# Optimization experiments

Hardware: AMD Instinct MI355X
Metric: run time of the kernel (lower is better)

## Reference

```python
import jax, jax.numpy as jnp
import numpy as np

B, H, S, D = 4, 16, 2048, 128

def setup_inputs() -> dict:
    key = jax.random.key(0)
    kq, kk, kv = jax.random.split(key, 3)
    query = jax.random.normal(kq, (B, H, S, D), dtype=jnp.float32)
    k = jax.random.normal(kk, (B, H, S, D), dtype=jnp.float32)
    v = jax.random.normal(kv, (B, H, S, D), dtype=jnp.float32)
    # causal mask: True = masked (not attended), broadcastable to (B,H,S,S)
    mask = jnp.triu(jnp.ones((S, S), dtype=bool), k=1)[None, None, :, :]
    return {"query": query, "key": k, "value": v, "mask": mask}

def reference(query, key, value, mask):
    d_k = query.shape[-1]
    scale = 1.0 / np.sqrt(d_k).astype(np.float32)
    # scores: (B,H,Sq,Sk)
    scores = jnp.einsum('bhqd,bhkd->bhqk', query, key) * scale
    scores = jnp.where(mask, -jnp.inf, scores)
    attention_weights = jax.nn.softmax(scores, axis=-1)
    output = jnp.einsum('bhqk,bhkd->bhqd', attention_weights, value)
    return output, attention_weights
```

## Files before the change

### kernel.cpp

```cpp
#include <hip/hip_runtime.h>
#include <hip/hip_bf16.h>

#define B_ 4
#define H_ 16
#define S_ 2048
#define D_ 128

typedef unsigned short u16;
typedef unsigned int u32;

typedef __attribute__((ext_vector_type(8))) short bf16x8;
typedef __attribute__((ext_vector_type(4))) float f32x4;
typedef __attribute__((ext_vector_type(4))) unsigned short u16x4;

__device__ __forceinline__ float bf2f(u16 x) {
    return __uint_as_float(((u32)x) << 16);
}

__device__ __forceinline__ u16 f2bf(float f) {
    u32 u = __float_as_uint(f);
    u32 lsb = (u >> 16) & 1u;
    u += 0x7fffu + lsb;
    return (u16)(u >> 16);
}

__global__ void detect_dtype_kernel(const u32* __restrict__ q, int* __restrict__ flag) {
    __shared__ int cnt;
    if (threadIdx.x == 0) cnt = 0;
    __syncthreads();
    int c = 0;
    for (int i = threadIdx.x; i < 4096; i += 256) {
        float lo = bf2f((u16)(q[i] & 0xffffu));
        if (!(fabsf(lo) <= 64.0f)) c++;
    }
    atomicAdd(&cnt, c);
    __syncthreads();
    if (threadIdx.x == 0) *flag = (cnt > 256) ? 1 : 0;
}

__global__ __launch_bounds__(256) void attn_bf16_kernel(
    const u16* __restrict__ Q, const u16* __restrict__ K, const u16* __restrict__ V,
    u16* __restrict__ Out, u16* __restrict__ W, const int* __restrict__ flag)
{
    if (*flag != 0) return;

    __shared__ float qs[D_];
    __shared__ float sc[S_];
    __shared__ float red[8];
    __shared__ float ot[512];

    const int tid = threadIdx.x;
    for (int idx = blockIdx.x; idx < B_ * H_ * S_; idx += (int)gridDim.x) {
        const int q   = idx & (S_ - 1);
        const int bh  = idx >> 11;
        const size_t rowQ = (size_t)idx * D_;
        const u16* Kb = K + (size_t)bh * S_ * D_;
        const u16* Vb = V + (size_t)bh * S_ * D_;
        const int nk = q + 1;
        const float scale = 0.08838834764831845f;

        if (tid < D_) qs[tid] = bf2f(Q[rowQ + tid]) * scale;
        __syncthreads();

        float lmax = -1e30f;
        for (int k = tid; k < nk; k += 256) {
            const uint4* K4 = reinterpret_cast<const uint4*>(Kb + (size_t)k * D_);
            float acc = 0.f;
            #pragma unroll
            for (int c = 0; c < D_ / 8; ++c) {
                uint4 u = K4[c];
                const int d = c * 8;
                acc += qs[d + 0] * bf2f((u16)(u.x & 0xffffu));
                acc += qs[d + 1] * bf2f((u16)(u.x >> 16));
                acc += qs[d + 2] * bf2f((u16)(u.y & 0xffffu));
                acc += qs[d + 3] * bf2f((u16)(u.y >> 16));
                acc += qs[d + 4] * bf2f((u16)(u.z & 0xffffu));
                acc += qs[d + 5] * bf2f((u16)(u.z >> 16));
                acc += qs[d + 6] * bf2f((u16)(u.w & 0xffffu));
                acc += qs[d + 7] * bf2f((u16)(u.w >> 16));
            }
            sc[k] = acc;
            lmax = fmaxf(lmax, acc);
        }

        #pragma unroll
        for (int off = 32; off > 0; off >>= 1)
            lmax = fmaxf(lmax, __shfl_down(lmax, off, 64));
        if ((tid & 63) == 0) red[tid >> 6] = lmax;
        __syncthreads();
        const float mx = fmaxf(fmaxf(red[0], red[1]), fmaxf(red[2], red[3]));

        float lsum = 0.f;
        for (int k = tid; k < nk; k += 256) {
            float e = __expf(sc[k] - mx);
            sc[k] = e;
            lsum += e;
        }
        #pragma unroll
        for (int off = 32; off > 0; off >>= 1)
            lsum += __shfl_down(lsum, off, 64);
        if ((tid & 63) == 0) red[4 + (tid >> 6)] = lsum;
        __syncthreads();
        const float rsum = 1.0f / (red[4] + red[5] + red[6] + red[7]);

        u32* Wrow2 = reinterpret_cast<u32*>(W + (size_t)idx * S_);
        for (int k2 = tid; k2 < S_ / 2; k2 += 256) {
            const int k0 = 2 * k2, k1 = 2 * k2 + 1;
            float w0 = (k0 < nk) ? sc[k0] * rsum : 0.f;
            float w1 = (k1 < nk) ? sc[k1] * rsum : 0.f;
            if (k0 < nk) sc[k0] = w0;
            if (k1 < nk) sc[k1] = w1;
            Wrow2[k2] = (u32)f2bf(w0) | ((u32)f2bf(w1) << 16);
        }
        __syncthreads();

        const int d2   = tid & 63;
        const int part = tid >> 6;
        const u32* V2 = reinterpret_cast<const u32*>(Vb);
        float a0 = 0.f, a1 = 0.f;
        for (int k = part; k < nk; k += 4) {
            const u32 u = V2[(size_t)k * (D_ / 2) + d2];
            const float w = sc[k];
            a0 += w * bf2f((u16)(u & 0xffffu));
            a1 += w * bf2f((u16)(u >> 16));
        }
        ot[part * D_ + 2 * d2]     = a0;
        ot[part * D_ + 2 * d2 + 1] = a1;
        __syncthreads();

        if (tid < D_) {
            const float o = ot[tid] + ot[D_ + tid] + ot[2 * D_ + tid] + ot[3 * D_ + tid];
            Out[rowQ + tid] = f2bf(o);
        }
        __syncthreads();
    }
}

__global__ __launch_bounds__(256) void split_qk_kernel(
    const float* __restrict__ Q, const float* __restrict__ K,
    u16* __restrict__ Qh, u16* __restrict__ Ql,
    u16* __restrict__ Kh, u16* __restrict__ Kl,
    const int* __restrict__ flag)
{
    if (*flag != 1) return;
    const float scale = 0.08838834764831845f;
    const int N4 = (B_ * H_ * S_ * D_) / 4;
    const float4* Q4 = reinterpret_cast<const float4*>(Q);
    const float4* K4 = reinterpret_cast<const float4*>(K);
    for (int g = blockIdx.x * 256 + threadIdx.x; g < N4; g += 2048 * 256) {
        {
            float4 v = Q4[g];
            float s0 = v.x * scale, s1 = v.y * scale, s2 = v.z * scale, s3 = v.w * scale;
            u16 h0 = f2bf(s0), h1 = f2bf(s1), h2 = f2bf(s2), h3 = f2bf(s3);
            u16x4 hv = {h0, h1, h2, h3};
            u16x4 lv = {f2bf(s0 - bf2f(h0)), f2bf(s1 - bf2f(h1)),
                        f2bf(s2 - bf2f(h2)), f2bf(s3 - bf2f(h3))};
            *reinterpret_cast<u16x4*>(&Qh[(size_t)4 * g]) = hv;
            *reinterpret_cast<u16x4*>(&Ql[(size_t)4 * g]) = lv;
        }
        {
            float4 v = K4[g];
            u16 h0 = f2bf(v.x), h1 = f2bf(v.y), h2 = f2bf(v.z), h3 = f2bf(v.w);
            u16x4 hv = {h0, h1, h2, h3};
            u16x4 lv = {f2bf(v.x - bf2f(h0)), f2bf(v.y - bf2f(h1)),
                        f2bf(v.z - bf2f(h2)), f2bf(v.w - bf2f(h3))};
            *reinterpret_cast<u16x4*>(&Kh[(size_t)4 * g]) = hv;
            *reinterpret_cast<u16x4*>(&Kl[(size_t)4 * g]) = lv;
        }
    }
}

__global__ __launch_bounds__(256) void transpose_v_kernel(
    const float* __restrict__ V, u16* __restrict__ VT, const int* __restrict__ flag)
{
    if (*flag != 1) return;
    __shared__ float ts[64 * 130];
    const int tid = threadIdx.x;
    const int bh = blockIdx.x >> 5;
    const int kt = blockIdx.x & 31;
    const int k0 = kt * 64;
    const float4* V4 = reinterpret_cast<const float4*>(V + ((size_t)bh * S_ + k0) * D_);
    #pragma unroll
    for (int it = 0; it < 8; ++it) {
        int g = tid + 256 * it;
        int r = g >> 5, c4 = g & 31;
        float4 v = V4[g];
        ts[r * 130 + 4 * c4 + 0] = v.x;
        ts[r * 130 + 4 * c4 + 1] = v.y;
        ts[r * 130 + 4 * c4 + 2] = v.z;
        ts[r * 130 + 4 * c4 + 3] = v.w;
    }
    __syncthreads();
    const int d = tid >> 1, kh2 = tid & 1;
    u16* dst = VT + (size_t)bh * (D_ * S_) + (size_t)d * S_ + k0 + 32 * kh2;
    #pragma unroll
    for (int jj = 0; jj < 4; ++jj) {
        bf16x8 o;
        #pragma unroll
        for (int j = 0; j < 8; ++j) {
            int k = 32 * kh2 + 8 * jj + j;
            o[j] = (short)f2bf(ts[k * 130 + d]);
        }
        *reinterpret_cast<bf16x8*>(&dst[8 * jj]) = o;
    }
}

#define ESTR 68

__global__ __launch_bounds__(256, 2) void attn_mfma_kernel(
    const u16* __restrict__ Qh, const u16* __restrict__ Ql,
    const u16* __restrict__ Kh, const u16* __restrict__ Kl,
    const u16* __restrict__ VT,
    float* __restrict__ Out, float* __restrict__ W, const int* __restrict__ flag)
{
    if (*flag != 1) return;

    __shared__ __align__(16) short qh_s[32 * 128];
    __shared__ __align__(16) short ql_s[32 * 128];
    __shared__ __align__(16) short kh_s[64 * 128];
    __shared__ __align__(16) short kl_s[64 * 128];
    __shared__ __align__(16) short vt_s[128 * 64];
    __shared__ __align__(16) float e_s[32 * ESTR];
    __shared__ float red2[2][32];
    __shared__ float rinv_s[32];

    const int tid = threadIdx.x;
    const int w   = tid >> 6;
    const int l   = tid & 63;
    const int l15 = l & 15;
    const int l4  = l >> 4;
    const int fq  = w >> 1;
    const int fk  = w & 1;

    const int bidx = blockIdx.x;
    const int bh   = bidx >> 6;
    const int qt   = 63 - (bidx & 63);
    const int q0   = qt << 5;
    const int nkt  = (q0 + 95) >> 6;

    const u16* QhB = Qh + ((size_t)bh * S_ + q0) * D_;
    const u16* QlB = Ql + ((size_t)bh * S_ + q0) * D_;
    const u16* KhB = Kh + (size_t)bh * S_ * D_;
    const u16* KlB = Kl + (size_t)bh * S_ * D_;
    const u16* VTB = VT + (size_t)bh * (size_t)D_ * S_;
    float* Ob = Out + ((size_t)bh * S_ + q0) * D_;
    float* Wb = W + ((size_t)bh * S_ + q0) * (size_t)S_;

    #pragma unroll
    for (int it = 0; it < 2; ++it) {
        int g = tid + 256 * it;
        int r = g >> 4, ch = g & 15;
        bf16x8 a = *reinterpret_cast<const bf16x8*>(&QhB[(size_t)r * D_ + 8 * ch]);
        bf16x8 b = *reinterpret_cast<const bf16x8*>(&QlB[(size_t)r * D_ + 8 * ch]);
        int li = r * 128 + ((8 * ch) ^ ((r & 7) << 3));
        *reinterpret_cast<bf16x8*>(&qh_s[li]) = a;
        *reinterpret_cast<bf16x8*>(&ql_s[li]) = b;
    }

    const int qrow = 16 * fq + l15;
    const int qx   = (qrow & 7) << 3;
    const int col0 = 8 * l4;

    f32x4 oacc[4];
    #pragma unroll
    for (int nb = 0; nb < 4; ++nb) { oacc[nb] = {0.f, 0.f, 0.f, 0.f}; }
    float rs[4] = {0.f, 0.f, 0.f, 0.f};

    bf16x8 rkh[4], rkl[4], rvt[4];
    {
        #pragma unroll
        for (int it = 0; it < 4; ++it) {
            int g = tid + 256 * it;
            rkh[it] = *reinterpret_cast<const bf16x8*>(&KhB[(size_t)(g >> 4) * D_ + 8 * (g & 15)]);
            rkl[it] = *reinterpret_cast<const bf16x8*>(&KlB[(size_t)(g >> 4) * D_ + 8 * (g & 15)]);
            rvt[it] = *reinterpret_cast<const bf16x8*>(&VTB[(size_t)(g >> 3) * S_ + 8 * (g & 7)]);
        }
    }

    for (int kt = 0; kt < nkt; ++kt) {
        const int k0 = kt << 6;

        #pragma unroll
        for (int it = 0; it < 4; ++it) {
            int g = tid + 256 * it;
            int r = g >> 4, ch = g & 15;
            int li = r * 128 + ((8 * ch) ^ ((r & 7) << 3));
            *reinterpret_cast<bf16x8*>(&kh_s[li]) = rkh[it];
            *reinterpret_cast<bf16x8*>(&kl_s[li]) = rkl[it];
            int d = g >> 3, c8 = g & 7;
            *reinterpret_cast<bf16x8*>(&vt_s[d * 64 + 8 * (c8 ^ (d & 7))]) = rvt[it];
        }
        __syncthreads();

        if (kt + 1 < nkt) {
            const int kn = k0 + 64;
            #pragma unroll
            for (int it = 0; it < 4; ++it) {
                int g = tid + 256 * it;
                rkh[it] = *reinterpret_cast<const bf16x8*>(&KhB[(size_t)(kn + (g >> 4)) * D_ + 8 * (g & 15)]);
                rkl[it] = *reinterpret_cast<const bf16x8*>(&KlB[(size_t)(kn + (g >> 4)) * D_ + 8 * (g & 15)]);
                rvt[it] = *reinterpret_cast<const bf16x8*>(&VTB[(size_t)(g >> 3) * S_ + kn + 8 * (g & 7)]);
            }
        }

        f32x4 acc2[2];
        acc2[0] = {0.f, 0.f, 0.f, 0.f};
        acc2[1] = {0.f, 0.f, 0.f, 0.f};
        #pragma unroll
        for (int nb = 0; nb < 2; ++nb) {
            const int krow = 32 * fk + 16 * nb + l15;
            const int kx   = (krow & 7) << 3;
            #pragma unroll
            for (int ks = 0; ks < 4; ++ks) {
                int ca = 32 * ks + col0;
                bf16x8 aH = *reinterpret_cast<const bf16x8*>(&qh_s[qrow * 128 + (ca ^ qx)]);
                bf16x8 aL = *reinterpret_cast<const bf16x8*>(&ql_s[qrow * 128 + (ca ^ qx)]);
                bf16x8 bH = *reinterpret_cast<const bf16x8*>(&kh_s[krow * 128 + (ca ^ kx)]);
                bf16x8 bL = *reinterpret_cast<const bf16x8*>(&kl_s[krow * 128 + (ca ^ kx)]);
                acc2[nb] = __builtin_amdgcn_mfma_f32_16x16x32_bf16(aH, bH, acc2[nb], 0, 0, 0);
                acc2[nb] = __builtin_amdgcn_mfma_f32_16x16x32_bf16(aH, bL, acc2[nb], 0, 0, 0);
                acc2[nb] = __builtin_amdgcn_mfma_f32_16x16x32_bf16(aL, bH, acc2[nb], 0, 0, 0);
            }
        }

        #pragma unroll
        for (int nb = 0; nb < 2; ++nb) {
            #pragma unroll
            for (int i = 0; i < 4; ++i) {
                int row = 16 * fq + 4 * l4 + i;
                int col = 32 * fk + 16 * nb + l15;
                float e = 0.f;
                if (k0 + col <= q0 + row) e = __expf(acc2[nb][i]);
                rs[i] += e;
                e_s[row * ESTR + col] = e;
            }
        }
        __syncthreads();

        #pragma unroll
        for (int t = 0; t < 2; ++t) {
            int idx = tid + 256 * t;
            int row = idx >> 4, c4 = idx & 15;
            f32x4 wv = *reinterpret_cast<const f32x4*>(&e_s[row * ESTR + 4 * c4]);
            *reinterpret_cast<f32x4*>(Wb + (size_t)row * S_ + k0 + 4 * c4) = wv;
        }

        #pragma unroll
        for (int ks2 = 0; ks2 < 2; ++ks2) {
            bf16x8 aP;
            {
                const float* pr = &e_s[(16 * fq + l15) * ESTR + 32 * ks2 + col0];
                float4 p0 = *reinterpret_cast<const float4*>(pr);
                float4 p1 = *reinterpret_cast<const float4*>(pr + 4);
                aP[0] = (short)f2bf(p0.x); aP[1] = (short)f2bf(p0.y);
                aP[2] = (short)f2bf(p0.z); aP[3] = (short)f2bf(p0.w);
                aP[4] = (short)f2bf(p1.x); aP[5] = (short)f2bf(p1.y);
                aP[6] = (short)f2bf(p1.z); aP[7] = (short)f2bf(p1.w);
            }
            #pragma unroll
            for (int nb = 0; nb < 4; ++nb) {
                int dcol = 64 * fk + 16 * nb + l15;
                bf16x8 bV = *reinterpret_cast<const bf16x8*>(
                    &vt_s[dcol * 64 + 8 * ((4 * ks2 + l4) ^ (dcol & 7))]);
                oacc[nb] = __builtin_amdgcn_mfma_f32_16x16x32_bf16(aP, bV, oacc[nb], 0, 0, 0);
            }
        }
        __syncthreads();
    }

    #pragma unroll
    for (int i = 0; i < 4; ++i) {
        float v = rs[i];
        v += __shfl_xor(v, 1, 64);
        v += __shfl_xor(v, 2, 64);
        v += __shfl_xor(v, 4, 64);
        v += __shfl_xor(v, 8, 64);
        if (l15 == 0) red2[fk][16 * fq + 4 * l4 + i] = v;
    }
    __syncthreads();
    if (tid < 32) rinv_s[tid] = 1.0f / (red2[0][tid] + red2[1][tid]);
    __syncthreads();

    #pragma unroll
    for (int nb = 0; nb < 4; ++nb) {
        #pragma unroll
        for (int i = 0; i < 4; ++i) {
            int row = 16 * fq + 4 * l4 + i;
            int col = 64 * fk + 16 * nb + l15;
            Ob[(size_t)row * D_ + col] = oacc[nb][i] * rinv_s[row];
        }
    }

    {
        const int kend = nkt << 6;
        f32x4* W4 = reinterpret_cast<f32x4*>(Wb);
        const f32x4 z4 = {0.f, 0.f, 0.f, 0.f};
        for (int g = tid; g < 32 * (S_ / 4); g += 256) {
            const int row = g >> 9;
            const int c4  = g & 511;
            const size_t off = (size_t)row * (S_ / 4) + c4;
            if ((c4 << 2) < kend) {
                f32x4 wv = W4[off];
                const float inv = rinv_s[row];
                wv.x *= inv; wv.y *= inv; wv.z *= inv; wv.w *= inv;
                W4[off] = wv;
            } else {
                __builtin_nontemporal_store(z4, &W4[off]);
            }
        }
    }
}

#define BQ 32
#define BK 64
#define LSTR 33
#define FESTR 68

__device__ __forceinline__ void dot4(float& a, const float4& x, const float4& y) {
    a = fmaf(x.x, y.x, a); a = fmaf(x.y, y.y, a);
    a = fmaf(x.z, y.z, a); a = fmaf(x.w, y.w, a);
}
__device__ __forceinline__ void fma4(float4& a, float s, const float4& b) {
    a.x = fmaf(s, b.x, a.x); a.y = fmaf(s, b.y, a.y);
    a.z = fmaf(s, b.z, a.z); a.w = fmaf(s, b.w, a.w);
}

__global__ __launch_bounds__(256) void attn_f32_tiled(
    const float* __restrict__ Q, const float* __restrict__ K, const float* __restrict__ V,
    float* __restrict__ Out, float* __restrict__ W, const int* __restrict__ flag)
{
    if (*flag != 1) return;

    __shared__ float4 qs4[BQ * LSTR];
    __shared__ float4 kv4[BK * LSTR];
    __shared__ __align__(16) float e_s[BQ * FESTR];
    __shared__ float rsum_s[BQ];
    __shared__ float rinv_s[BQ];

    const int tid  = threadIdx.x;
    const int bidx = blockIdx.x;
    const int bh   = bidx >> 6;
    const int qt   = 63 - (bidx & 63);
    const int q0   = qt << 5;
    const int nkt  = ((q0 + BQ - 1) >> 6) + 1;
    const float scale = 0.08838834764831845f;

    const float* Kb = K + (size_t)bh * (S_ * D_);
    const float* Vb = V + (size_t)bh * (S_ * D_);
    const float* Qb = Q + ((size_t)bh * S_ + q0) * D_;
    float* Ob = Out + ((size_t)bh * S_ + q0) * D_;
    float* Wb = W + ((size_t)bh * S_ + q0) * (size_t)S_;

    const int rgq = tid >> 4;
    const int cgq = tid & 15;
    const int rg = tid >> 4;
    const int cg = tid & 15;

    {
        const float4* Qg = reinterpret_cast<const float4*>(Qb);
        #pragma unroll
        for (int t = 0; t < 4; ++t) {
            const int g = tid + 256 * t;
            qs4[(g >> 5) * LSTR + (g & 31)] = Qg[g];
        }
        const float4* Kg = reinterpret_cast<const float4*>(Kb);
        #pragma unroll
        for (int t = 0; t < 8; ++t) {
            const int g = tid + 256 * t;
            kv4[(g >> 5) * LSTR + (g & 31)] = Kg[g];
        }
    }
    __syncthreads();

    float4 o4[2][2] = {};
    float rsf[2] = {0.f, 0.f};

    for (int kt = 0; kt < nkt; ++kt) {
        const int k0 = kt << 6;
        const bool more = (kt + 1 < nkt);

        float4 vreg[8];
        {
            const float4* Vg = reinterpret_cast<const float4*>(Vb) + (size_t)k0 * 32;
            #pragma unroll
            for (int t = 0; t < 8; ++t) vreg[t] = Vg[tid + 256 * t];
        }

        float acc[2][4] = {};
        {
            const int qb0 = (rgq * 2 + 0) * LSTR;
            const int qb1 = (rgq * 2 + 1) * LSTR;
            const int kb0 = (cgq +  0) * LSTR;
            const int kb1 = (cgq + 16) * LSTR;
            const int kb2 = (cgq + 32) * LSTR;
            const int kb3 = (cgq + 48) * LSTR;
            #pragma unroll 4
            for (int d4 = 0; d4 < 32; ++d4) {
                const float4 qv0 = qs4[qb0 + d4];
                const float4 qv1 = qs4[qb1 + d4];
                const float4 kv0 = kv4[kb0 + d4];
                const float4 kv1 = kv4[kb1 + d4];
                const float4 kv2 = kv4[kb2 + d4];
                const float4 kv3 = kv4[kb3 + d4];
                dot4(acc[0][0], qv0, kv0); dot4(acc[0][1], qv0, kv1);
                dot4(acc[0][2], qv0, kv2); dot4(acc[0][3], qv0, kv3);
                dot4(acc[1][0], qv1, kv0); dot4(acc[1][1], qv1, kv1);
                dot4(acc[1][2], qv1, kv2); dot4(acc[1][3], qv1, kv3);
            }
        }

        #pragma unroll
        for (int i = 0; i < 2; ++i) {
            const int r  = rgq * 2 + i;
            const int qg = q0 + r;
            float* Wrow = Wb + (size_t)r * S_ + k0;
            #pragma unroll
            for (int j = 0; j < 4; ++j) {
                const int kc = cgq + 16 * j;
                const float e = (k0 + kc <= qg) ? __expf(acc[i][j] * scale) : 0.0f;
                rsf[i] += e;
                e_s[r * FESTR + kc] = e;
                Wrow[kc] = e;
            }
        }
        __syncthreads();

        #pragma unroll
        for (int t = 0; t < 8; ++t) {
            const int g = tid + 256 * t;
            kv4[(g >> 5) * LSTR + (g & 31)] = vreg[t];
        }
        float4 kreg[8];
        if (more) {
            const float4* Kg = reinterpret_cast<const float4*>(Kb) + (size_t)(k0 + BK) * 32;
            #pragma unroll
            for (int t = 0; t < 8; ++t) kreg[t] = Kg[tid + 256 * t];
        }
        __syncthreads();

        {
            const int eb0 = (rg * 2 + 0) * FESTR;
            const int eb1 = (rg * 2 + 1) * FESTR;
            #pragma unroll 2
            for (int kk = 0; kk < BK; kk += 4) {
                const float4 e0 = *reinterpret_cast<const float4*>(&e_s[eb0 + kk]);
                const float4 e1 = *reinterpret_cast<const float4*>(&e_s[eb1 + kk]);
                const float ea[4] = {e0.x, e0.y, e0.z, e0.w};
                const float eb[4] = {e1.x, e1.y, e1.z, e1.w};
                #pragma unroll
                for (int t = 0; t < 4; ++t) {
                    const float4 v0 = kv4[(kk + t) * LSTR + cg];
                    const float4 v1 = kv4[(kk + t) * LSTR + 16 + cg];
                    fma4(o4[0][0], ea[t], v0);
                    fma4(o4[0][1], ea[t], v1);
                    fma4(o4[1][0], eb[t], v0);
                    fma4(o4[1][1], eb[t], v1);
                }
            }
        }

        if (more) {
            __syncthreads();
            #pragma unroll
            for (int t = 0; t < 8; ++t) {
                const int g = tid + 256 * t;
                kv4[(g >> 5) * LSTR + (g & 31)] = kreg[t];
            }
            __syncthreads();
        }
    }

    #pragma unroll
    for (int i = 0; i < 2; ++i) {
        float v = rsf[i];
        v += __shfl_xor(v, 8, 64);
        v += __shfl_xor(v, 4, 64);
        v += __shfl_xor(v, 2, 64);
        v += __shfl_xor(v, 1, 64);
        if (cgq == 0) rsum_s[rgq * 2 + i] = v;
    }
    __syncthreads();
    if (tid < BQ) rinv_s[tid] = 1.0f / rsum_s[tid];
    __syncthreads();

    #pragma unroll
    for (int i = 0; i < 2; ++i) {
        const int r = rg * 2 + i;
        const float inv = rinv_s[r];
        float4 a = o4[i][0];
        a.x *= inv; a.y *= inv; a.z *= inv; a.w *= inv;
        float4 b = o4[i][1];
        b.x *= inv; b.y *= inv; b.z *= inv; b.w *= inv;
        float4* Orow = reinterpret_cast<float4*>(Ob + (size_t)r * D_);
        Orow[cg]      = a;
        Orow[16 + cg] = b;
    }

    {
        const int kend = nkt << 6;
        float4* W4 = reinterpret_cast<float4*>(Wb);
        for (int g = tid; g < BQ * (S_ / 4); g += 256) {
            const int row = g >> 9;
            const int c4  = g & 511;
            const size_t off = (size_t)row * (S_ / 4) + c4;
            if ((c4 << 2) < kend) {
                float4 wv = W4[off];
                const float inv = rinv_s[row];
                wv.x *= inv; wv.y *= inv; wv.z *= inv; wv.w *= inv;
                W4[off] = wv;
            } else {
                W4[off] = make_float4(0.f, 0.f, 0.f, 0.f);
            }
        }
    }
}

extern "C" void kernel_launch(void* const* d_in, const int* in_sizes, int n_in,
                              void* d_out, int out_size, void* d_ws, size_t ws_size,
                              hipStream_t stream) {
    int* flag = (int*)d_ws;

    detect_dtype_kernel<<<dim3(1), dim3(256), 0, stream>>>((const u32*)d_in[0], flag);

    {
        const u16* Q = (const u16*)d_in[0];
        const u16* K = (const u16*)d_in[1];
        const u16* V = (const u16*)d_in[2];
        u16* Out = (u16*)d_out;
        u16* Wp  = Out + (size_t)B_ * H_ * S_ * D_;
        attn_bf16_kernel<<<dim3(2048), dim3(256), 0, stream>>>(Q, K, V, Out, Wp, flag);
    }

    const size_t PLSZ = (size_t)B_ * H_ * S_ * D_;
    const size_t NEED = 256 + 5 * PLSZ * sizeof(u16);
    float* OutF = (float*)d_out;
    float* WF   = OutF + PLSZ;

    if (ws_size >= NEED) {
        u16* base = (u16*)((char*)d_ws + 256);
        u16* Qh = base;
        u16* Ql = Qh + PLSZ;
        u16* Kh = Ql + PLSZ;
        u16* Kl = Kh + PLSZ;
        u16* VTp = Kl + PLSZ;
        split_qk_kernel<<<dim3(2048), dim3(256), 0, stream>>>(
            (const float*)d_in[0], (const float*)d_in[1], Qh, Ql, Kh, Kl, flag);
        transpose_v_kernel<<<dim3(2048), dim3(256), 0, stream>>>(
            (const float*)d_in[2], VTp, flag);
        attn_mfma_kernel<<<dim3(B_ * H_ * (S_ / 32)), dim3(256), 0, stream>>>(
            Qh, Ql, Kh, Kl, VTp, OutF, WF, flag);
    } else {
        attn_f32_tiled<<<dim3(B_ * H_ * (S_ / 32)), dim3(256), 0, stream>>>(
            (const float*)d_in[0], (const float*)d_in[1], (const float*)d_in[2],
            OutF, WF, flag);
    }
}
```

Before: 1.918 ms.

## Make each wave own 16 query rows and read K/V directly from global

Each 256-thread block now covers 64 query rows, and each wave independently handles 16 of them. Q fragments are held in registers, and K and V^T fragments are loaded straight from global memory (relying on cache) instead of being staged cooperatively through shared memory. Per-wave shared memory is used only for the exp tile, so block-wide __syncthreads are removed and LDS use drops sharply. In exchange, the four waves each fetch the same K/V tiles from global/L2 without sharing, and the prefetch double-buffering is gone. The launch grid is halved to match the larger query tile.

```diff
diff --git a/kernel.cpp b/kernel.cpp
--- a/kernel.cpp
+++ b/kernel.cpp
@@ -215,141 +215,90 @@
 {
     if (*flag != 1) return;
 
-    __shared__ __align__(16) short qh_s[32 * 128];
-    __shared__ __align__(16) short ql_s[32 * 128];
-    __shared__ __align__(16) short kh_s[64 * 128];
-    __shared__ __align__(16) short kl_s[64 * 128];
-    __shared__ __align__(16) short vt_s[128 * 64];
-    __shared__ __align__(16) float e_s[32 * ESTR];
-    __shared__ float red2[2][32];
-    __shared__ float rinv_s[32];
+    __shared__ __align__(16) float e_s[4][16 * ESTR];
 
     const int tid = threadIdx.x;
-    const int w   = tid >> 6;
+    const int wv  = tid >> 6;
     const int l   = tid & 63;
     const int l15 = l & 15;
     const int l4  = l >> 4;
-    const int fq  = w >> 1;
-    const int fk  = w & 1;
 
     const int bidx = blockIdx.x;
-    const int bh   = bidx >> 6;
-    const int qt   = 63 - (bidx & 63);
-    const int q0   = qt << 5;
-    const int nkt  = (q0 + 95) >> 6;
-
-    const u16* QhB = Qh + ((size_t)bh * S_ + q0) * D_;
-    const u16* QlB = Ql + ((size_t)bh * S_ + q0) * D_;
+    const int bh   = bidx >> 5;
+    const int qt   = 31 - (bidx & 31);
+    const int q0   = qt << 6;
+    const int nkt  = qt + 1;
+    const int qw   = q0 + 16 * wv;
+
+    const u16* QhW = Qh + ((size_t)bh * S_ + qw) * D_;
+    const u16* QlW = Ql + ((size_t)bh * S_ + qw) * D_;
     const u16* KhB = Kh + (size_t)bh * S_ * D_;
     const u16* KlB = Kl + (size_t)bh * S_ * D_;
     const u16* VTB = VT + (size_t)bh * (size_t)D_ * S_;
-    float* Ob = Out + ((size_t)bh * S_ + q0) * D_;
-    float* Wb = W + ((size_t)bh * S_ + q0) * (size_t)S_;
-
-    #pragma unroll
-    for (int it = 0; it < 2; ++it) {
-        int g = tid + 256 * it;
-        int r = g >> 4, ch = g & 15;
-        bf16x8 a = *reinterpret_cast<const bf16x8*>(&QhB[(size_t)r * D_ + 8 * ch]);
-        bf16x8 b = *reinterpret_cast<const bf16x8*>(&QlB[(size_t)r * D_ + 8 * ch]);
-        int li = r * 128 + ((8 * ch) ^ ((r & 7) << 3));
-        *reinterpret_cast<bf16x8*>(&qh_s[li]) = a;
-        *reinterpret_cast<bf16x8*>(&ql_s[li]) = b;
-    }
-
-    const int qrow = 16 * fq + l15;
-    const int qx   = (qrow & 7) << 3;
-    const int col0 = 8 * l4;
-
-    f32x4 oacc[4];
-    #pragma unroll
-    for (int nb = 0; nb < 4; ++nb) { oacc[nb] = {0.f, 0.f, 0.f, 0.f}; }
+    float* Ob = Out + ((size_t)bh * S_ + qw) * D_;
+    float* Wb = W + ((size_t)bh * S_ + qw) * (size_t)S_;
+
+    float* ew = e_s[wv];
+
+    bf16x8 aH[4], aL[4];
+    #pragma unroll
+    for (int ks = 0; ks < 4; ++ks) {
+        aH[ks] = *reinterpret_cast<const bf16x8*>(&QhW[(size_t)l15 * D_ + 32 * ks + 8 * l4]);
+        aL[ks] = *reinterpret_cast<const bf16x8*>(&QlW[(size_t)l15 * D_ + 32 * ks + 8 * l4]);
+    }
+
+    f32x4 oacc[8];
+    #pragma unroll
+    for (int nb = 0; nb < 8; ++nb) { oacc[nb] = {0.f, 0.f, 0.f, 0.f}; }
     float rs[4] = {0.f, 0.f, 0.f, 0.f};
-
-    bf16x8 rkh[4], rkl[4], rvt[4];
-    {
-        #pragma unroll
-        for (int it = 0; it < 4; ++it) {
-            int g = tid + 256 * it;
-            rkh[it] = *reinterpret_cast<const bf16x8*>(&KhB[(size_t)(g >> 4) * D_ + 8 * (g & 15)]);
-            rkl[it] = *reinterpret_cast<const bf16x8*>(&KlB[(size_t)(g >> 4) * D_ + 8 * (g & 15)]);
-            rvt[it] = *reinterpret_cast<const bf16x8*>(&VTB[(size_t)(g >> 3) * S_ + 8 * (g & 7)]);
-        }
-    }
 
     for (int kt = 0; kt < nkt; ++kt) {
         const int k0 = kt << 6;
 
-        #pragma unroll
-        for (int it = 0; it < 4; ++it) {
-            int g = tid + 256 * it;
-            int r = g >> 4, ch = g & 15;
-            int li = r * 128 + ((8 * ch) ^ ((r & 7) << 3));
-            *reinterpret_cast<bf16x8*>(&kh_s[li]) = rkh[it];
-            *reinterpret_cast<bf16x8*>(&kl_s[li]) = rkl[it];
-            int d = g >> 3, c8 = g & 7;
-            *reinterpret_cast<bf16x8*>(&vt_s[d * 64 + 8 * (c8 ^ (d & 7))]) = rvt[it];
-        }
-        __syncthreads();
-
-        if (kt + 1 < nkt) {
-            const int kn = k0 + 64;
-            #pragma unroll
-            for (int it = 0; it < 4; ++it) {
-                int g = tid + 256 * it;
-                rkh[it] = *reinterpret_cast<const bf16x8*>(&KhB[(size_t)(kn + (g >> 4)) * D_ + 8 * (g & 15)]);
-                rkl[it] = *reinterpret_cast<const bf16x8*>(&KlB[(size_t)(kn + (g >> 4)) * D_ + 8 * (g & 15)]);
-                rvt[it] = *reinterpret_cast<const bf16x8*>(&VTB[(size_t)(g >> 3) * S_ + kn + 8 * (g & 7)]);
-            }
-        }
-
-        f32x4 acc2[2];
-        acc2[0] = {0.f, 0.f, 0.f, 0.f};
-        acc2[1] = {0.f, 0.f, 0.f, 0.f};
-        #pragma unroll
-        for (int nb = 0; nb < 2; ++nb) {
-            const int krow = 32 * fk + 16 * nb + l15;
-            const int kx   = (krow & 7) << 3;
+        f32x4 sc[4];
+        #pragma unroll
+        for (int nb = 0; nb < 4; ++nb) {
+            const u16* khp = KhB + (size_t)(k0 + 16 * nb + l15) * D_ + 8 * l4;
+            const u16* klp = KlB + (size_t)(k0 + 16 * nb + l15) * D_ + 8 * l4;
+            f32x4 accA = {0.f, 0.f, 0.f, 0.f};
+            f32x4 accB = {0.f, 0.f, 0.f, 0.f};
             #pragma unroll
             for (int ks = 0; ks < 4; ++ks) {
-                int ca = 32 * ks + col0;
-                bf16x8 aH = *reinterpret_cast<const bf16x8*>(&qh_s[qrow * 128 + (ca ^ qx)]);
-                bf16x8 aL = *reinterpret_cast<const bf16x8*>(&ql_s[qrow * 128 + (ca ^ qx)]);
-                bf16x8 bH = *reinterpret_cast<const bf16x8*>(&kh_s[krow * 128 + (ca ^ kx)]);
-                bf16x8 bL = *reinterpret_cast<const bf16x8*>(&kl_s[krow * 128 + (ca ^ kx)]);
-                acc2[nb] = __builtin_amdgcn_mfma_f32_16x16x32_bf16(aH, bH, acc2[nb], 0, 0, 0);
-                acc2[nb] = __builtin_amdgcn_mfma_f32_16x16x32_bf16(aH, bL, acc2[nb], 0, 0, 0);
-                acc2[nb] = __builtin_amdgcn_mfma_f32_16x16x32_bf16(aL, bH, acc2[nb], 0, 0, 0);
-            }
-        }
-
-        #pragma unroll
-        for (int nb = 0; nb < 2; ++nb) {
+                bf16x8 bH = *reinterpret_cast<const bf16x8*>(khp + 32 * ks);
+                bf16x8 bL = *reinterpret_cast<const bf16x8*>(klp + 32 * ks);
+                accA = __builtin_amdgcn_mfma_f32_16x16x32_bf16(aH[ks], bH, accA, 0, 0, 0);
+                accB = __builtin_amdgcn_mfma_f32_16x16x32_bf16(aH[ks], bL, accB, 0, 0, 0);
+                accB = __builtin_amdgcn_mfma_f32_16x16x32_bf16(aL[ks], bH, accB, 0, 0, 0);
+            }
+            sc[nb] = accA + accB;
+        }
+
+        #pragma unroll
+        for (int nb = 0; nb < 4; ++nb) {
             #pragma unroll
             for (int i = 0; i < 4; ++i) {
-                int row = 16 * fq + 4 * l4 + i;
-                int col = 32 * fk + 16 * nb + l15;
+                const int row  = 4 * l4 + i;
+                const int colg = k0 + 16 * nb + l15;
                 float e = 0.f;
-                if (k0 + col <= q0 + row) e = __expf(acc2[nb][i]);
+                if (colg <= qw + row) e = __expf(sc[nb][i]);
                 rs[i] += e;
-                e_s[row * ESTR + col] = e;
-            }
-        }
-        __syncthreads();
-
-        #pragma unroll
-        for (int t = 0; t < 2; ++t) {
-            int idx = tid + 256 * t;
-            int row = idx >> 4, c4 = idx & 15;
-            f32x4 wv = *reinterpret_cast<const f32x4*>(&e_s[row * ESTR + 4 * c4]);
-            *reinterpret_cast<f32x4*>(Wb + (size_t)row * S_ + k0 + 4 * c4) = wv;
+                ew[row * ESTR + 16 * nb + l15] = e;
+            }
+        }
+
+        #pragma unroll
+        for (int t = 0; t < 4; ++t) {
+            const int g = t * 64 + l;
+            const int r = g >> 4, c4 = g & 15;
+            f32x4 wvv = *reinterpret_cast<const f32x4*>(&ew[r * ESTR + 4 * c4]);
+            *reinterpret_cast<f32x4*>(Wb + (size_t)r * S_ + k0 + 4 * c4) = wvv;
         }
 
         #pragma unroll
         for (int ks2 = 0; ks2 < 2; ++ks2) {
             bf16x8 aP;
             {
-                const float* pr = &e_s[(16 * fq + l15) * ESTR + 32 * ks2 + col0];
+                const float* pr = &ew[l15 * ESTR + 32 * ks2 + 8 * l4];
                 float4 p0 = *reinterpret_cast<const float4*>(pr);
                 float4 p1 = *reinterpret_cast<const float4*>(pr + 4);
                 aP[0] = (short)f2bf(p0.x); aP[1] = (short)f2bf(p0.y);
@@ -358,16 +307,15 @@
                 aP[6] = (short)f2bf(p1.z); aP[7] = (short)f2bf(p1.w);
             }
             #pragma unroll
-            for (int nb = 0; nb < 4; ++nb) {
-                int dcol = 64 * fk + 16 * nb + l15;
-                bf16x8 bV = *reinterpret_cast<const bf16x8*>(
-                    &vt_s[dcol * 64 + 8 * ((4 * ks2 + l4) ^ (dcol & 7))]);
-                oacc[nb] = __builtin_amdgcn_mfma_f32_16x16x32_bf16(aP, bV, oacc[nb], 0, 0, 0);
-            }
-        }
-        __syncthreads();
-    }
-
+            for (int nb2 = 0; nb2 < 8; ++nb2) {
+                const u16* vp = VTB + (size_t)(16 * nb2 + l15) * S_ + k0 + 32 * ks2 + 8 * l4;
+                bf16x8 bV = *reinterpret_cast<const bf16x8*>(vp);
+                oacc[nb2] = __builtin_amdgcn_mfma_f32_16x16x32_bf16(aP, bV, oacc[nb2], 0, 0, 0);
+            }
+        }
+    }
+
+    float rinv[4];
     #pragma unroll
     for (int i = 0; i < 4; ++i) {
         float v = rs[i];
@@ -375,37 +323,37 @@
         v += __shfl_xor(v, 2, 64);
         v += __shfl_xor(v, 4, 64);
         v += __shfl_xor(v, 8, 64);
-        if (l15 == 0) red2[fk][16 * fq + 4 * l4 + i] = v;
-    }
-    __syncthreads();
-    if (tid < 32) rinv_s[tid] = 1.0f / (red2[0][tid] + red2[1][tid]);
-    __syncthreads();
-
-    #pragma unroll
-    for (int nb = 0; nb < 4; ++nb) {
+        rinv[i] = 1.0f / v;
+        ew[(4 * l4 + i) * ESTR + 64] = rinv[i];
+    }
+
+    #pragma unroll
+    for (int nb2 = 0; nb2 < 8; ++nb2) {
         #pragma unroll
         for (int i = 0; i < 4; ++i) {
-            int row = 16 * fq + 4 * l4 + i;
-            int col = 64 * fk + 16 * nb + l15;
-            Ob[(size_t)row * D_ + col] = oacc[nb][i] * rinv_s[row];
+            const int row = 4 * l4 + i;
+            Ob[(size_t)row * D_ + 16 * nb2 + l15] = oacc[nb2][i] * rinv[i];
         }
     }
 
     {
-        const int kend = nkt << 6;
+        const int kend4 = nkt << 4;
         f32x4* W4 = reinterpret_cast<f32x4*>(Wb);
         const f32x4 z4 = {0.f, 0.f, 0.f, 0.f};
-        for (int g = tid; g < 32 * (S_ / 4); g += 256) {
-            const int row = g >> 9;
-            const int c4  = g & 511;
-            const size_t off = (size_t)row * (S_ / 4) + c4;
-            if ((c4 << 2) < kend) {
-                f32x4 wv = W4[off];
-                const float inv = rinv_s[row];
-                wv.x *= inv; wv.y *= inv; wv.z *= inv; wv.w *= inv;
-                W4[off] = wv;
-            } else {
-                __builtin_nontemporal_store(z4, &W4[off]);
+        #pragma unroll 2
+        for (int r = 0; r < 16; ++r) {
+            const float inv = ew[r * ESTR + 64];
+            #pragma unroll
+            for (int t = 0; t < 8; ++t) {
+                const int c4 = l + 64 * t;
+                const size_t off = (size_t)r * (S_ / 4) + c4;
+                if (c4 < kend4) {
+                    f32x4 wvv = W4[off];
+                    wvv.x *= inv; wvv.y *= inv; wvv.z *= inv; wvv.w *= inv;
+                    W4[off] = wvv;
+                } else {
+                    __builtin_nontemporal_store(z4, &W4[off]);
+                }
             }
         }
     }
@@ -647,7 +595,7 @@
             (const float*)d_in[0], (const float*)d_in[1], Qh, Ql, Kh, Kl, flag);
         transpose_v_kernel<<<dim3(2048), dim3(256), 0, stream>>>(
             (const float*)d_in[2], VTp, flag);
-        attn_mfma_kernel<<<dim3(B_ * H_ * (S_ / 32)), dim3(256), 0, stream>>>(
+        attn_mfma_kernel<<<dim3(B_ * H_ * (S_ / 64)), dim3(256), 0, stream>>>(
             Qh, Ql, Kh, Kl, VTp, OutF, WF, flag);
     } else {
         attn_f32_tiled<<<dim3(B_ * H_ * (S_ / 32)), dim3(256), 0, stream>>>(
```

Result: slower. 2.969 ms (+54.8%).
